# Performance work log

Hardware: AMD Instinct MI355X
Metric: run time of the kernel (lower is better)

Reference implementation:

```python
import jax, jax.numpy as jnp
import numpy as np

B, SEQ, DIM = 2, 4096, 1024
E, S = 8, 512          # num_slots = seq_len // num_experts
HID = 4 * DIM          # FeedForward hidden: dim * mult
SCALE = DIM ** 0.5     # RMSNorm scale


def rmsnorm(x, gamma):
    # matches F.normalize(x, dim=-1) * dim**0.5 * gamma (eps=1e-12 clamp on the norm)
    n = jnp.linalg.norm(x, axis=-1, keepdims=True)
    return x / jnp.maximum(n, 1e-12) * SCALE * gamma


def setup_inputs() -> dict:
    key = jax.random.key(0)
    ks = jax.random.split(key, 4)
    w_init = lambda k, shape: jax.random.normal(k, shape, dtype=jnp.float32) * 0.02
    return {
        "x": jax.random.normal(ks[0], (B, SEQ, DIM), dtype=jnp.float32),
        "norm_gamma": jnp.ones((DIM,), jnp.float32),
        "slot_norm_gamma": jnp.ones((DIM,), jnp.float32),
        "slot_embeds": jax.random.normal(ks[1], (E, S, DIM), dtype=jnp.float32),
        "w1": w_init(ks[2], (E, DIM, HID)),
        "b1": jnp.zeros((E, HID), jnp.float32),
        "w2": w_init(ks[3], (E, HID, DIM)),
        "b2": jnp.zeros((E, DIM), jnp.float32),
    }


def reference(x, norm_gamma, slot_norm_gamma, slot_embeds, w1, b1, w2, b2):
    xn = rmsnorm(x, norm_gamma)                 # [b, n, d]
    sn = rmsnorm(slot_embeds, slot_norm_gamma)  # [e, s, d]

    logits = jnp.einsum('bnd,esd->bnes', xn, sn)                   # [b, n, e, s]
    dispatch = jax.nn.softmax(logits, axis=1)                      # softmax over tokens n
    b, n, e, s = logits.shape
    combine = jax.nn.softmax(logits.reshape(b, n, e * s), axis=-1) # softmax over (e s)

    slots = jnp.einsum('bnd,bnes->besd', xn, dispatch)             # [b, e, s, d]

    # per-expert FeedForward: Linear -> GELU(exact) -> Linear (dropout=0)
    h = jnp.einsum('besd,edh->besh', slots, w1) + b1[None, :, None, :]
    h = jax.nn.gelu(h, approximate=False)
    eo = jnp.einsum('besh,ehd->besd', h, w2) + b2[None, :, None, :]

    eo = eo.reshape(b, e * s, DIM)                                 # [b, (e s), d]
    out = jnp.einsum('bmd,bnm->bnd', eo, combine)                  # [b, n, d]
    return out
```

## Files before the change

kernel.cpp:

```cpp
#include <hip/hip_runtime.h>
#include <math.h>

#define SEQ    4096
#define DIM    1024
#define NEXP   8
#define NSLOT  512
#define ES     4096
#define HID    4096
#define NB     2
#define RMS_SCALE 32.0f

typedef __attribute__((ext_vector_type(4))) float f32x4;
typedef __attribute__((ext_vector_type(8))) short bf16x8;
typedef __attribute__((ext_vector_type(4))) unsigned short us4;

__device__ __forceinline__ unsigned short f2bf(float f) {
    unsigned u = __float_as_uint(f);
    u += 0x7fff + ((u >> 16) & 1);
    return (unsigned short)(u >> 16);
}
__device__ __forceinline__ float bf2f(unsigned short h) {
    return __uint_as_float(((unsigned)h) << 16);
}
__device__ __forceinline__ float gelu_exact(float x) {
    return 0.5f * x * (1.0f + erff(x * 0.70710678118654752f));
}

#define GLOAD_LDS16(gp, lp) \
    __builtin_amdgcn_global_load_lds((const __attribute__((address_space(1))) void*)(gp), \
                                     (__attribute__((address_space(3))) void*)(lp), 16, 0, 0)

__device__ __forceinline__ unsigned ldsoff(const void* p) {
    return (unsigned)(size_t)(const __attribute__((address_space(3))) void*)p;
}

#define DSR(dst, base, off) asm volatile("ds_read_b128 %0, %1 offset:" off : "=v"(dst) : "v"(base))
#define VM(n) asm volatile("s_waitcnt vmcnt(" #n ")" ::: "memory")
#define BAR __builtin_amdgcn_s_barrier()
#define SCB __builtin_amdgcn_sched_barrier(0)

#define PH_OPEN  SCB; BAR; asm volatile("s_waitcnt lgkmcnt(0)" ::: "memory"); SCB; \
                 __builtin_amdgcn_s_setprio(1);
#define PH_CLOSE __builtin_amdgcn_s_setprio(0); SCB;

__global__ void rmsnorm_split(const float* __restrict__ in, const float* __restrict__ gamma,
                              unsigned short* __restrict__ outc) {
    int row = blockIdx.x;
    int t = threadIdx.x;
    float4 v = reinterpret_cast<const float4*>(in + (size_t)row * DIM)[t];
    float ss = v.x*v.x + v.y*v.y + v.z*v.z + v.w*v.w;
    #pragma unroll
    for (int off = 32; off >= 1; off >>= 1) ss += __shfl_down(ss, off, 64);
    __shared__ float red[4];
    if ((t & 63) == 0) red[t >> 6] = ss;
    __syncthreads();
    float inv = RMS_SCALE / fmaxf(sqrtf(red[0] + red[1] + red[2] + red[3]), 1e-12f);
    float4 g = reinterpret_cast<const float4*>(gamma)[t];
    float f[4] = {v.x*inv*g.x, v.y*inv*g.y, v.z*inv*g.z, v.w*inv*g.w};
    us4 hv, lv;
    #pragma unroll
    for (int q = 0; q < 4; ++q) {
        unsigned short h = f2bf(f[q]);
        hv[q] = h;
        lv[q] = f2bf(f[q] - bf2f(h));
    }
    unsigned short* rb = outc + (size_t)row * 2048;
    *reinterpret_cast<us4*>(&rb[t*4]) = hv;
    *reinterpret_cast<us4*>(&rb[1024 + t*4]) = lv;
}

__global__ void rowmax_reduce(const float* __restrict__ pM, float* __restrict__ rmax) {
    int row = blockIdx.x * 256 + threadIdx.x;
    float m = -INFINITY;
    for (int p = 0; p < 64; ++p) m = fmaxf(m, pM[(size_t)p*8192 + row]);
    rmax[row] = m;
}
__global__ void colmax_reduce(const float* __restrict__ pM, float* __restrict__ cmax) {
    int col = blockIdx.x * 256 + threadIdx.x;
    int b = blockIdx.y;
    float m = -INFINITY;
    for (int p = b*32; p < b*32 + 32; ++p) m = fmaxf(m, pM[(size_t)p*4096 + col]);
    cmax[b*4096 + col] = m;
}
__global__ void sum_reduce(const float* __restrict__ pS, float* __restrict__ sinv) {
    int fl = blockIdx.x * 256 + threadIdx.x;
    float s = 0.f;
    for (int p = 0; p < 128; ++p) s += pS[(size_t)p*8192 + fl];
    sinv[fl] = 1.0f / s;
}

__global__ void make_weights(const float* __restrict__ logits,
                             const float* __restrict__ cmax, const float* __restrict__ rmax,
                             unsigned short* __restrict__ comb, unsigned short* __restrict__ dispT,
                             float* __restrict__ rowpS, float* __restrict__ colpS) {
    int b = blockIdx.z;
    const float* L = logits + (size_t)b * SEQ * ES;
    int n0 = blockIdx.y * 32, e0 = blockIdx.x * 32;
    int t = threadIdx.x;
    int r = t >> 3, c4 = (t & 7) * 4;
    __shared__ unsigned short tile[32][36];
    float4 v = *reinterpret_cast<const float4*>(&L[(size_t)(n0 + r) * ES + e0 + c4]);
    float rm = rmax[b*SEQ + n0 + r];
    float vv[4] = {v.x, v.y, v.z, v.w};
    us4 cb;
    float rs = 0.f;
    #pragma unroll
    for (int q = 0; q < 4; ++q) {
        cb[q] = f2bf(__expf(vv[q] - rm));
        rs += bf2f(cb[q]);
        float dv = __expf(vv[q] - cmax[b*ES + e0 + c4 + q]);
        tile[c4 + q][r] = f2bf(dv);
    }
    *reinterpret_cast<us4*>(&comb[(size_t)b*SEQ*ES + (size_t)(n0 + r)*ES + e0 + c4]) = cb;
    rs += __shfl_xor(rs, 1, 64);
    rs += __shfl_xor(rs, 2, 64);
    rs += __shfl_xor(rs, 4, 64);
    if ((t & 7) == 0)
        rowpS[(size_t)blockIdx.x * 8192 + b*SEQ + n0 + r] = rs;
    __syncthreads();
    us4 o = *reinterpret_cast<us4*>(&tile[t >> 3][(t & 7) * 4]);
    *reinterpret_cast<us4*>(&dispT[(size_t)b*ES*SEQ + (size_t)(e0 + (t >> 3))*SEQ + n0 + (t & 7)*4]) = o;
    float cs = bf2f(o[0]) + bf2f(o[1]) + bf2f(o[2]) + bf2f(o[3]);
    cs += __shfl_xor(cs, 1, 64);
    cs += __shfl_xor(cs, 2, 64);
    cs += __shfl_xor(cs, 4, 64);
    if ((t & 7) == 0)
        colpS[(size_t)blockIdx.y * 8192 + b*ES + e0 + (t >> 3)] = cs;
}

__global__ void transpose_b16(const unsigned short* __restrict__ src, unsigned short* __restrict__ dst,
                              int sld, int dld, long sStride, long dStride) {
    int z = blockIdx.z;
    const unsigned short* S = src + (size_t)z * sStride;
    unsigned short* D = dst + (size_t)z * dStride;
    int r0 = blockIdx.y * 32, c0 = blockIdx.x * 32;
    int t = threadIdx.x;
    __shared__ unsigned short tile[32][36];
    us4 v = *reinterpret_cast<const us4*>(&S[(size_t)(r0 + (t>>3)) * sld + c0 + (t&7)*4]);
    #pragma unroll
    for (int q = 0; q < 4; ++q) tile[(t&7)*4 + q][t>>3] = v[q];
    __syncthreads();
    us4 o = *reinterpret_cast<us4*>(&tile[t >> 3][(t & 7) * 4]);
    *reinterpret_cast<us4*>(&D[(size_t)(c0 + (t>>3)) * dld + r0 + (t&7)*4]) = o;
}

__global__ void transpose_f32_b16(const float* __restrict__ src, unsigned short* __restrict__ dst,
                                  int sld, int dld, long sStride, long dStride) {
    int z = blockIdx.z;
    const float* S = src + (size_t)z * sStride;
    unsigned short* D = dst + (size_t)z * dStride;
    int r0 = blockIdx.y * 32, c0 = blockIdx.x * 32;
    int t = threadIdx.x;
    __shared__ unsigned short tile[32][36];
    float4 v = *reinterpret_cast<const float4*>(&S[(size_t)(r0 + (t>>3)) * sld + c0 + (t&7)*4]);
    float vv[4] = {v.x, v.y, v.z, v.w};
    #pragma unroll
    for (int q = 0; q < 4; ++q) tile[(t&7)*4 + q][t>>3] = f2bf(vv[q]);
    __syncthreads();
    us4 o = *reinterpret_cast<us4*>(&tile[t >> 3][(t & 7) * 4]);
    *reinterpret_cast<us4*>(&D[(size_t)(c0 + (t>>3)) * dld + r0 + (t&7)*4]) = o;
}

template<int EPI, int OM, int STATS, int SPLIT>
__global__ __launch_bounds__(512, 2)
void mfma_gemm256(const unsigned short* __restrict__ A, const unsigned short* __restrict__ B,
                  void* __restrict__ Cv, const float* __restrict__ bias,
                  int N, int K, int lda, int ldb, int ldc,
                  long aStride, long bStride, long cStride, int bMod,
                  float* __restrict__ rowpM, float* __restrict__ colpM) {
    __shared__ unsigned short lds[65536];
    const int t = threadIdx.x;
    const int lane = t & 63, wave = t >> 6;
    const int wr = wave >> 2, wc = wave & 3;
    const int z = blockIdx.z, zb = z % bMod;
    const unsigned short* Ab = A + (size_t)z * aStride;
    const unsigned short* Bb = B + (size_t)zb * bStride;
    const int gx = gridDim.x;
    int flat = blockIdx.x + blockIdx.y * gx;
    const int cpx = (gx * gridDim.y) >> 3;
    flat = (flat & 7) * cpx + (flat >> 3);
    const int m0 = (flat / gx) * 256, n0 = (flat % gx) * 256;

    const int sr = t >> 3;
    const int sg = (t & 7) ^ (sr & 7);
    const unsigned short* gA = Ab + (size_t)(m0 + sr) * lda + sg * 8;
    const unsigned short* gB = Bb + (size_t)(n0 + sr) * ldb + sg * 8;
    unsigned short* ldsw = lds + wave * 512;

    const int lr = lane & 15, lk = lane >> 4;
    const unsigned sw0 = (unsigned)(((lk)     ^ (lr & 7)) << 4);
    const unsigned sw1 = (unsigned)(((4 + lk) ^ (lr & 7)) << 4);
    const unsigned l0  = ldsoff(lds);
    const unsigned arow = (unsigned)((wr*128 + lr) * 128);
    const unsigned brow = (unsigned)((wc*64  + lr) * 128);
    const unsigned ab00 = l0 + arow + sw0,          ab10 = l0 + arow + sw1;
    const unsigned bb00 = l0 + 32768 + brow + sw0,  bb10 = l0 + 32768 + brow + sw1;
    const unsigned ab01 = ab00 + 65536, ab11 = ab10 + 65536;
    const unsigned bb01 = bb00 + 65536, bb11 = bb10 + 65536;

    #define KOA(tt) ((size_t)((SPLIT && (tt) >= 16) ? ((tt)-16)*64 : (tt)*64))
    #define KOB(tt) ((size_t)((SPLIT && (tt) >= 32) ? ((tt)-32)*64 : (tt)*64))

    #define STAGE_A(buf, half, tt) do { \
        const unsigned short* _g = gA + (size_t)((half)*128) * lda + KOA(tt); \
        unsigned short* _l = ldsw + (buf)*32768 + (half)*8192; \
        GLOAD_LDS16(_g, _l); \
        GLOAD_LDS16(_g + (size_t)64*lda, _l + 4096); } while(0)
    #define STAGE_B(buf, half, tt) do { \
        const unsigned short* _g = gB + (size_t)((half)*128) * ldb + KOB(tt); \
        unsigned short* _l = ldsw + (buf)*32768 + 16384 + (half)*8192; \
        GLOAD_LDS16(_g, _l); \
        GLOAD_LDS16(_g + (size_t)64*ldb, _l + 4096); } while(0)

    #define MFMA16(MB, CN) \
        _Pragma("unroll") \
        for (int m = 0; m < 4; ++m) { \
            _Pragma("unroll") \
            for (int n = 0; n < 2; ++n) { \
                acc[(MB)+m][(CN)+n] = __builtin_amdgcn_mfma_f32_16x16x32_bf16(a0[m], b0[(CN)+n], acc[(MB)+m][(CN)+n], 0, 0, 0); \
                acc[(MB)+m][(CN)+n] = __builtin_amdgcn_mfma_f32_16x16x32_bf16(a1[m], b1[(CN)+n], acc[(MB)+m][(CN)+n], 0, 0, 0); \
            } \
        }

    f32x4 acc[8][4] = {};
    bf16x8 a0[4], a1[4], b0[4], b1[4];
    const int NT = K / 64;

    STAGE_B(0, 0, 0); STAGE_B(0, 1, 0);
    STAGE_A(0, 0, 0); STAGE_A(0, 1, 0);
    STAGE_B(1, 0, 1); STAGE_B(1, 1, 1);
    VM(4); BAR;

    for (int tt = 0; tt < NT; tt += 2) {
        const bool pf = (tt + 2 < NT);
        DSR(a0[0], ab00, "0");    DSR(a0[1], ab00, "2048");
        DSR(a0[2], ab00, "4096"); DSR(a0[3], ab00, "6144");
        DSR(a1[0], ab10, "0");    DSR(a1[1], ab10, "2048");
        DSR(a1[2], ab10, "4096"); DSR(a1[3], ab10, "6144");
        DSR(b0[0], bb00, "0");    DSR(b0[1], bb00, "2048");
        DSR(b1[0], bb10, "0");    DSR(b1[1], bb10, "2048");
        STAGE_A(1, 0, tt+1);
        PH_OPEN MFMA16(0, 0) PH_CLOSE
        BAR;
        DSR(b0[2], bb00, "4096"); DSR(b0[3], bb00, "6144");
        DSR(b1[2], bb10, "4096"); DSR(b1[3], bb10, "6144");
        STAGE_A(1, 1, tt+1);
        PH_OPEN MFMA16(0, 2) PH_CLOSE
        BAR;
        DSR(a0[0], ab00, "8192");  DSR(a0[1], ab00, "10240");
        DSR(a0[2], ab00, "12288"); DSR(a0[3], ab00, "14336");
        DSR(a1[0], ab10, "8192");  DSR(a1[1], ab10, "10240");
        DSR(a1[2], ab10, "12288"); DSR(a1[3], ab10, "14336");
        if (pf) STAGE_B(0, 0, tt+2);
        PH_OPEN MFMA16(4, 0) PH_CLOSE
        BAR;
        if (pf) STAGE_B(0, 1, tt+2);
        PH_OPEN MFMA16(4, 2) PH_CLOSE
        if (pf) { VM(4); } else { VM(0); }
        BAR;
        DSR(a0[0], ab01, "0");    DSR(a0[1], ab01, "2048");
        DSR(a0[2], ab01, "4096"); DSR(a0[3], ab01, "6144");
        DSR(a1[0], ab11, "0");    DSR(a1[1], ab11, "2048");
        DSR(a1[2], ab11, "4096"); DSR(a1[3], ab11, "6144");
        DSR(b0[0], bb01, "0");    DSR(b0[1], bb01, "2048");
        DSR(b1[0], bb11, "0");    DSR(b1[1], bb11, "2048");
        if (pf) STAGE_A(0, 0, tt+2);
        PH_OPEN MFMA16(0, 0) PH_CLOSE
        BAR;
        DSR(b0[2], bb01, "4096"); DSR(b0[3], bb01, "6144");
        DSR(b1[2], bb11, "4096"); DSR(b1[3], bb11, "6144");
        if (pf) STAGE_A(0, 1, tt+2);
        PH_OPEN MFMA16(0, 2) PH_CLOSE
        BAR;
        DSR(a0[0], ab01, "8192");  DSR(a0[1], ab01, "10240");
        DSR(a0[2], ab01, "12288"); DSR(a0[3], ab01, "14336");
        DSR(a1[0], ab11, "8192");  DSR(a1[1], ab11, "10240");
        DSR(a1[2], ab11, "12288"); DSR(a1[3], ab11, "14336");
        if (pf) STAGE_B(1, 0, tt+3);
        PH_OPEN MFMA16(4, 0) PH_CLOSE
        BAR;
        if (pf) STAGE_B(1, 1, tt+3);
        PH_OPEN MFMA16(4, 2) PH_CLOSE
        if (pf) { VM(4); } else { VM(0); }
        BAR;
    }

    if (STATS) {
        #pragma unroll
        for (int f = 0; f < 8; ++f) {
            #pragma unroll
            for (int r = 0; r < 4; ++r) {
                float m = fmaxf(fmaxf(acc[f][0][r], acc[f][1][r]), fmaxf(acc[f][2][r], acc[f][3][r]));
                #pragma unroll
                for (int msk = 1; msk <= 8; msk <<= 1) m = fmaxf(m, __shfl_xor(m, msk, 64));
                if ((lane & 15) == 0) {
                    int row = m0 + wr*128 + f*16 + (lane>>4)*4 + r;
                    int slot = (n0 >> 6) + wc;
                    rowpM[(size_t)slot*8192 + row] = m;
                }
            }
        }
        #pragma unroll
        for (int n = 0; n < 4; ++n) {
            float m = -INFINITY;
            #pragma unroll
            for (int f = 0; f < 8; ++f)
                #pragma unroll
                for (int r = 0; r < 4; ++r) m = fmaxf(m, acc[f][n][r]);
            m = fmaxf(m, __shfl_xor(m, 16, 64));
            m = fmaxf(m, __shfl_xor(m, 32, 64));
            if ((lane >> 4) == 0) {
                int col = n0 + wc*64 + n*16 + lane;
                int slot = (m0 >> 7) + wr;
                colpM[(size_t)slot*4096 + col] = m;
            }
        }
    }

    const float* bz = (EPI != 0) ? bias + (size_t)zb * N : nullptr;
    long coff = (long)z * cStride;
    int rbase = (lane >> 4) * 4;
    int cbase = lane & 15;
    #pragma unroll
    for (int f = 0; f < 8; ++f) {
        #pragma unroll
        for (int n = 0; n < 4; ++n) {
            int col  = n0 + wc*64 + n*16 + cbase;
            int row0 = m0 + wr*128 + f*16 + rbase;
            float bv = (EPI != 0) ? bz[col] : 0.f;
            float vals[4];
            #pragma unroll
            for (int r = 0; r < 4; ++r) {
                float v = acc[f][n][r] + bv;
                if (EPI == 2) v = gelu_exact(v);
                vals[r] = v;
            }
            if (OM == 0) {
                float* C = (float*)Cv + coff;
                #pragma unroll
                for (int r = 0; r < 4; ++r) C[(size_t)(row0 + r) * ldc + col] = vals[r];
            } else {
                unsigned short* C = (unsigned short*)Cv + coff;
                #pragma unroll
                for (int r = 0; r < 4; ++r) C[(size_t)(row0 + r) * ldc + col] = f2bf(vals[r]);
            }
        }
    }
    #undef STAGE_A
    #undef STAGE_B
    #undef MFMA16
    #undef KOA
    #undef KOB
}

template<int EPI, int OM, int SC>
__global__ __launch_bounds__(512, 2)
void mfma_gemmX(const unsigned short* __restrict__ A, const unsigned short* __restrict__ B,
                void* __restrict__ Cv, const float* __restrict__ bias,
                int N, int K, int lda, int ldb, int ldc,
                long aStride, long bStride, long cStride, long cStrideE, int bMod,
                const float* __restrict__ svec) {
    __shared__ unsigned short lds[49152];
    const int t = threadIdx.x;
    const int lane = t & 63, wave = t >> 6;
    const int wr = wave >> 2, wc = wave & 3;
    const int z = blockIdx.z, zb = z % bMod;
    const unsigned short* Ab = A + (size_t)z * aStride;
    const unsigned short* Bb = B + (size_t)zb * bStride;
    const int gx = gridDim.x;
    int flat = blockIdx.x + blockIdx.y * gx;
    const int cpx = (gx * gridDim.y) >> 3;
    flat = (flat & 7) * cpx + (flat >> 3);
    const int m0 = (flat / gx) * 256, n0 = (flat % gx) * 128;

    const int sr = t >> 3;
    const int sg = (t & 7) ^ (sr & 7);
    const unsigned short* gA = Ab + (size_t)(m0 + sr) * lda + sg * 8;
    const unsigned short* gB = Bb + (size_t)(n0 + sr) * ldb + sg * 8;
    unsigned short* ldsw = lds + wave * 512;

    const int lr = lane & 15, lk = lane >> 4;
    const unsigned g0 = (unsigned)(((lk)     ^ (lr & 7)) << 4);
    const unsigned g1 = (unsigned)(((4 + lk) ^ (lr & 7)) << 4);
    const unsigned l0 = ldsoff(lds);
    const unsigned arow = (unsigned)((wr*64 + lr) * 128);
    const unsigned brow = (unsigned)((wc*32 + lr) * 128);
    const unsigned ax00 = l0 + arow + g0,          ax10 = l0 + arow + g1;
    const unsigned bx00 = l0 + 32768 + brow + g0,  bx10 = l0 + 32768 + brow + g1;
    const unsigned ax01 = ax00 + 49152, ax11 = ax10 + 49152;
    const unsigned bx01 = bx00 + 49152, bx11 = bx10 + 49152;

    #define STAGE_AX(buf, quad, tt) do { \
        const unsigned short* _g = gA + (size_t)((quad)*64) * lda + (tt)*64; \
        unsigned short* _l = ldsw + (buf)*24576 + (quad)*8192; \
        GLOAD_LDS16(_g, _l); \
        GLOAD_LDS16(_g + (size_t)128*lda, _l + 4096); } while(0)
    #define STAGE_BX(buf, tt) do { \
        const unsigned short* _g = gB + (tt)*64; \
        unsigned short* _l = ldsw + (buf)*24576 + 16384; \
        GLOAD_LDS16(_g, _l); \
        GLOAD_LDS16(_g + (size_t)64*ldb, _l + 4096); } while(0)

    #define MFMA8(MB, AR, BR) \
        _Pragma("unroll") \
        for (int m = 0; m < 4; ++m) { \
            _Pragma("unroll") \
            for (int n = 0; n < 2; ++n) { \
                acc[(MB)+m][n] = __builtin_amdgcn_mfma_f32_16x16x32_bf16(AR[m], BR[n], acc[(MB)+m][n], 0, 0, 0); \
            } \
        }

    f32x4 acc[8][2] = {};
    bf16x8 a0[4], a1[4], b0[2], b1[2];
    const int NT = K / 64;

    STAGE_AX(0, 0, 0); STAGE_BX(0, 0); STAGE_AX(0, 1, 0);
    STAGE_AX(1, 0, 1); STAGE_BX(1, 1);
    VM(0); BAR;

    for (int tt = 0; tt < NT; tt += 2) {
        const bool pf2 = (tt + 2 < NT);
        const bool pf3 = (tt + 3 < NT);
        DSR(a0[0], ax00, "0");    DSR(a0[1], ax00, "2048");
        DSR(a0[2], ax00, "4096"); DSR(a0[3], ax00, "6144");
        DSR(b0[0], bx00, "0");    DSR(b0[1], bx00, "2048");
        STAGE_AX(1, 1, tt+1);
        PH_OPEN MFMA8(0, a0, b0) PH_CLOSE
        BAR;
        DSR(a1[0], ax10, "0");    DSR(a1[1], ax10, "2048");
        DSR(a1[2], ax10, "4096"); DSR(a1[3], ax10, "6144");
        DSR(b1[0], bx10, "0");    DSR(b1[1], bx10, "2048");
        PH_OPEN MFMA8(0, a1, b1) PH_CLOSE
        BAR;
        DSR(a0[0], ax00, "16384"); DSR(a0[1], ax00, "18432");
        DSR(a0[2], ax00, "20480"); DSR(a0[3], ax00, "22528");
        if (pf2) STAGE_AX(0, 0, tt+2);
        PH_OPEN MFMA8(4, a0, b0) PH_CLOSE
        BAR;
        DSR(a1[0], ax10, "16384"); DSR(a1[1], ax10, "18432");
        DSR(a1[2], ax10, "20480"); DSR(a1[3], ax10, "22528");
        if (pf2) STAGE_BX(0, tt+2);
        PH_OPEN MFMA8(4, a1, b1) PH_CLOSE
        if (pf2) { VM(4); } else { VM(0); }
        BAR;
        DSR(a0[0], ax01, "0");    DSR(a0[1], ax01, "2048");
        DSR(a0[2], ax01, "4096"); DSR(a0[3], ax01, "6144");
        DSR(b0[0], bx01, "0");    DSR(b0[1], bx01, "2048");
        if (pf2) STAGE_AX(0, 1, tt+2);
        PH_OPEN MFMA8(0, a0, b0) PH_CLOSE
        BAR;
        DSR(a1[0], ax11, "0");    DSR(a1[1], ax11, "2048");
        DSR(a1[2], ax11, "4096"); DSR(a1[3], ax11, "6144");
        DSR(b1[0], bx11, "0");    DSR(b1[1], bx11, "2048");
        PH_OPEN MFMA8(0, a1, b1) PH_CLOSE
        BAR;
        DSR(a0[0], ax01, "16384"); DSR(a0[1], ax01, "18432");
        DSR(a0[2], ax01, "20480"); DSR(a0[3], ax01, "22528");
        if (pf3) STAGE_AX(1, 0, tt+3);
        PH_OPEN MFMA8(4, a0, b0) PH_CLOSE
        BAR;
        DSR(a1[0], ax11, "16384"); DSR(a1[1], ax11, "18432");
        DSR(a1[2], ax11, "20480"); DSR(a1[3], ax11, "22528");
        if (pf3) STAGE_BX(1, tt+3);
        PH_OPEN MFMA8(4, a1, b1) PH_CLOSE
        if (pf3) { VM(4); } else { VM(0); }
        BAR;
    }

    const float* bz = (EPI != 0) ? bias + (size_t)zb * N : nullptr;
    const float* sv = SC ? svec + (size_t)z * 4096 : nullptr;
    long coff = (long)z * cStride + (long)zb * cStrideE;
    int rbase = (lane >> 4) * 4;
    int cbase = lane & 15;
    #pragma unroll
    for (int f = 0; f < 8; ++f) {
        #pragma unroll
        for (int n = 0; n < 2; ++n) {
            int col  = n0 + wc*32 + n*16 + cbase;
            int row0 = m0 + wr*128 + f*16 + rbase;
            float bv = (EPI != 0) ? bz[col] : 0.f;
            float vals[4];
            #pragma unroll
            for (int r = 0; r < 4; ++r) {
                float v = acc[f][n][r] + bv;
                if (SC) v *= sv[row0 + r];
                if (EPI == 2) v = gelu_exact(v);
                vals[r] = v;
            }
            if (OM == 0) {
                float* C = (float*)Cv + coff;
                #pragma unroll
                for (int r = 0; r < 4; ++r) C[(size_t)(row0 + r) * ldc + col] = vals[r];
            } else if (OM == 1) {
                unsigned short* C = (unsigned short*)Cv + coff;
                #pragma unroll
                for (int r = 0; r < 4; ++r) C[(size_t)(row0 + r) * ldc + col] = f2bf(vals[r]);
            } else {
                unsigned short* C = (unsigned short*)Cv + coff;
                us4 o;
                #pragma unroll
                for (int r = 0; r < 4; ++r) o[r] = f2bf(vals[r]);
                *reinterpret_cast<us4*>(&C[(size_t)col * ldc + row0]) = o;
            }
        }
    }
    #undef STAGE_AX
    #undef STAGE_BX
    #undef MFMA8
}

extern "C" void kernel_launch(void* const* d_in, const int* in_sizes, int n_in,
                              void* d_out, int out_size, void* d_ws, size_t ws_size,
                              hipStream_t stream) {
    const float* x    = (const float*)d_in[0];
    const float* ng   = (const float*)d_in[1];
    const float* sg   = (const float*)d_in[2];
    const float* semb = (const float*)d_in[3];
    const float* w1   = (const float*)d_in[4];
    const float* b1   = (const float*)d_in[5];
    const float* w2   = (const float*)d_in[6];
    const float* b2   = (const float*)d_in[7];
    float* out = (float*)d_out;

    char* base = (char*)d_ws;
    unsigned short* Acat  = (unsigned short*)(base);
    unsigned short* Bcat  = (unsigned short*)(base + 33554432);
    unsigned short* dispT = (unsigned short*)(base);
    unsigned short* w2T   = (unsigned short*)(base);
    float*          logits= (float*)(base + 75497472);
    unsigned short* hbuf  = (unsigned short*)(base + 75497472);
    unsigned short* w1T   = (unsigned short*)(base + 142606336);
    unsigned short* xnT   = (unsigned short*)(base + 209715200);
    unsigned short* comb  = (unsigned short*)(base + 226492416);
    unsigned short* slots = (unsigned short*)(base + 293601280);
    unsigned short* eoT   = (unsigned short*)(base + 293601280);
    float* rowpM = (float*)(base + 226492416);
    float* colpM = rowpM + 64*8192;
    float* rmax  = (float*)(base + 310378496);
    float* rinv  = rmax + 8192;
    float* cmax  = rinv + 8192;
    float* cinv  = cmax + 8192;
    float* rowpS = cinv + 8192;
    float* colpS = rowpS + 128*8192;

    rmsnorm_split<<<NB*SEQ, 256, 0, stream>>>(x, ng, Acat);
    rmsnorm_split<<<NEXP*NSLOT, 256, 0, stream>>>(semb, sg, Bcat);

    transpose_b16<<<dim3(DIM/32, SEQ/32, NB), 256, 0, stream>>>(
        Acat, xnT, 2048, SEQ, (long)SEQ*2048, (long)DIM*SEQ);

    mfma_gemm256<0,0,1,1><<<dim3(ES/256, (NB*SEQ)/256, 1), 512, 0, stream>>>(
        Acat, Bcat, logits, nullptr, ES, 3072, 2048, 2048, ES,
        0L, 0L, 0L, 1, rowpM, colpM);

    rowmax_reduce<<<32, 256, 0, stream>>>(rowpM, rmax);
    colmax_reduce<<<dim3(16, 2), 256, 0, stream>>>(colpM, cmax);

    make_weights<<<dim3(ES/32, SEQ/32, NB), 256, 0, stream>>>(
        logits, cmax, rmax, comb, dispT, rowpS, colpS);

    sum_reduce<<<32, 256, 0, stream>>>(rowpS, rinv);
    sum_reduce<<<32, 256, 0, stream>>>(colpS, cinv);

    transpose_f32_b16<<<dim3(HID/32, DIM/32, NEXP), 256, 0, stream>>>(
        w1, w1T, HID, DIM, (long)DIM*HID, (long)HID*DIM);

    mfma_gemmX<0,1,1><<<dim3(DIM/128, ES/256, NB), 512, 0, stream>>>(
        dispT, xnT, slots, nullptr, DIM, SEQ, SEQ, SEQ, DIM,
        (long)ES*SEQ, (long)DIM*SEQ, (long)ES*DIM, 0L, NB, cinv);

    transpose_f32_b16<<<dim3(DIM/32, HID/32, NEXP), 256, 0, stream>>>(
        w2, w2T, DIM, HID, (long)HID*DIM, (long)DIM*HID);

    mfma_gemm256<2,1,0,0><<<dim3(HID/256, NSLOT/256, NB*NEXP), 512, 0, stream>>>(
        slots, w1T, hbuf, b1, HID, DIM, DIM, DIM, HID,
        (long)NSLOT*DIM, (long)HID*DIM, (long)NSLOT*HID, NEXP,
        nullptr, nullptr);

    mfma_gemmX<1,2,0><<<dim3(DIM/128, NSLOT/256, NB*NEXP), 512, 0, stream>>>(
        hbuf, w2T, eoT, b2, DIM, HID, HID, HID, ES,
        (long)NSLOT*HID, (long)DIM*HID, (long)(DIM*ES/NEXP), (long)(NSLOT - DIM*ES/NEXP), NEXP,
        nullptr);

    mfma_gemmX<0,0,1><<<dim3(DIM/128, SEQ/256, NB), 512, 0, stream>>>(
        comb, eoT, out, nullptr, DIM, ES, ES, ES, DIM,
        (long)SEQ*ES, (long)DIM*ES, (long)SEQ*DIM, 0L, NB, rinv);
}
```

Baseline: 700.9 us.

## Switch GEMMs from bf16 to fp16 and shorten split-precision logits K

Replaces bf16 storage and MFMA instructions with fp16 throughout, and changes the logits GEMM's split-precision scheme. The x operand is still split into hi and lo halves, but the slot operand now duplicates its hi part, so K drops from 3072 to 2048 (x_hi·s_hi + x_lo·s_hi). This removes a third of the logits GEMM work by relying on fp16's extra mantissa bits for slot embeddings. The trade-off is fp16's narrower exponent range, which risks overflow or underflow in the exp values, hidden activations and weights.

```diff
diff --git a/kernel.cpp b/kernel.cpp
--- a/kernel.cpp
+++ b/kernel.cpp
@@ -11,16 +11,18 @@
 #define RMS_SCALE 32.0f
 
 typedef __attribute__((ext_vector_type(4))) float f32x4;
-typedef __attribute__((ext_vector_type(8))) short bf16x8;
+typedef __attribute__((ext_vector_type(8))) _Float16 f16x8;
 typedef __attribute__((ext_vector_type(4))) unsigned short us4;
 
-__device__ __forceinline__ unsigned short f2bf(float f) {
-    unsigned u = __float_as_uint(f);
-    u += 0x7fff + ((u >> 16) & 1);
-    return (unsigned short)(u >> 16);
-}
-__device__ __forceinline__ float bf2f(unsigned short h) {
-    return __uint_as_float(((unsigned)h) << 16);
+__device__ __forceinline__ unsigned short f2h(float f) {
+    union { _Float16 h; unsigned short u; } c;
+    c.h = (_Float16)f;
+    return c.u;
+}
+__device__ __forceinline__ float h2f(unsigned short u) {
+    union { unsigned short u; _Float16 h; } c;
+    c.u = u;
+    return (float)c.h;
 }
 __device__ __forceinline__ float gelu_exact(float x) {
     return 0.5f * x * (1.0f + erff(x * 0.70710678118654752f));
@@ -43,6 +45,7 @@
                  __builtin_amdgcn_s_setprio(1);
 #define PH_CLOSE __builtin_amdgcn_s_setprio(0); SCB;
 
+template<int ORDER>
 __global__ void rmsnorm_split(const float* __restrict__ in, const float* __restrict__ gamma,
                               unsigned short* __restrict__ outc) {
     int row = blockIdx.x;
@@ -60,9 +63,9 @@
     us4 hv, lv;
     #pragma unroll
     for (int q = 0; q < 4; ++q) {
-        unsigned short h = f2bf(f[q]);
+        unsigned short h = f2h(f[q]);
         hv[q] = h;
-        lv[q] = f2bf(f[q] - bf2f(h));
+        lv[q] = (ORDER == 0) ? f2h(f[q] - h2f(h)) : h;
     }
     unsigned short* rb = outc + (size_t)row * 2048;
     *reinterpret_cast<us4*>(&rb[t*4]) = hv;
@@ -106,10 +109,10 @@
     float rs = 0.f;
     #pragma unroll
     for (int q = 0; q < 4; ++q) {
-        cb[q] = f2bf(__expf(vv[q] - rm));
-        rs += bf2f(cb[q]);
+        cb[q] = f2h(__expf(vv[q] - rm));
+        rs += h2f(cb[q]);
         float dv = __expf(vv[q] - cmax[b*ES + e0 + c4 + q]);
-        tile[c4 + q][r] = f2bf(dv);
+        tile[c4 + q][r] = f2h(dv);
     }
     *reinterpret_cast<us4*>(&comb[(size_t)b*SEQ*ES + (size_t)(n0 + r)*ES + e0 + c4]) = cb;
     rs += __shfl_xor(rs, 1, 64);
@@ -120,7 +123,7 @@
     __syncthreads();
     us4 o = *reinterpret_cast<us4*>(&tile[t >> 3][(t & 7) * 4]);
     *reinterpret_cast<us4*>(&dispT[(size_t)b*ES*SEQ + (size_t)(e0 + (t >> 3))*SEQ + n0 + (t & 7)*4]) = o;
-    float cs = bf2f(o[0]) + bf2f(o[1]) + bf2f(o[2]) + bf2f(o[3]);
+    float cs = h2f(o[0]) + h2f(o[1]) + h2f(o[2]) + h2f(o[3]);
     cs += __shfl_xor(cs, 1, 64);
     cs += __shfl_xor(cs, 2, 64);
     cs += __shfl_xor(cs, 4, 64);
@@ -144,7 +147,7 @@
     *reinterpret_cast<us4*>(&D[(size_t)(c0 + (t>>3)) * dld + r0 + (t&7)*4]) = o;
 }
 
-__global__ void transpose_f32_b16(const float* __restrict__ src, unsigned short* __restrict__ dst,
+__global__ void transpose_f32_h16(const float* __restrict__ src, unsigned short* __restrict__ dst,
                                   int sld, int dld, long sStride, long dStride) {
     int z = blockIdx.z;
     const float* S = src + (size_t)z * sStride;
@@ -155,13 +158,13 @@
     float4 v = *reinterpret_cast<const float4*>(&S[(size_t)(r0 + (t>>3)) * sld + c0 + (t&7)*4]);
     float vv[4] = {v.x, v.y, v.z, v.w};
     #pragma unroll
-    for (int q = 0; q < 4; ++q) tile[(t&7)*4 + q][t>>3] = f2bf(vv[q]);
+    for (int q = 0; q < 4; ++q) tile[(t&7)*4 + q][t>>3] = f2h(vv[q]);
     __syncthreads();
     us4 o = *reinterpret_cast<us4*>(&tile[t >> 3][(t & 7) * 4]);
     *reinterpret_cast<us4*>(&D[(size_t)(c0 + (t>>3)) * dld + r0 + (t&7)*4]) = o;
 }
 
-template<int EPI, int OM, int STATS, int SPLIT>
+template<int EPI, int OM, int STATS>
 __global__ __launch_bounds__(512, 2)
 void mfma_gemm256(const unsigned short* __restrict__ A, const unsigned short* __restrict__ B,
                   void* __restrict__ Cv, const float* __restrict__ bias,
@@ -198,16 +201,13 @@
     const unsigned ab01 = ab00 + 65536, ab11 = ab10 + 65536;
     const unsigned bb01 = bb00 + 65536, bb11 = bb10 + 65536;
 
-    #define KOA(tt) ((size_t)((SPLIT && (tt) >= 16) ? ((tt)-16)*64 : (tt)*64))
-    #define KOB(tt) ((size_t)((SPLIT && (tt) >= 32) ? ((tt)-32)*64 : (tt)*64))
-
     #define STAGE_A(buf, half, tt) do { \
-        const unsigned short* _g = gA + (size_t)((half)*128) * lda + KOA(tt); \
+        const unsigned short* _g = gA + (size_t)((half)*128) * lda + (size_t)(tt)*64; \
         unsigned short* _l = ldsw + (buf)*32768 + (half)*8192; \
         GLOAD_LDS16(_g, _l); \
         GLOAD_LDS16(_g + (size_t)64*lda, _l + 4096); } while(0)
     #define STAGE_B(buf, half, tt) do { \
-        const unsigned short* _g = gB + (size_t)((half)*128) * ldb + KOB(tt); \
+        const unsigned short* _g = gB + (size_t)((half)*128) * ldb + (size_t)(tt)*64; \
         unsigned short* _l = ldsw + (buf)*32768 + 16384 + (half)*8192; \
         GLOAD_LDS16(_g, _l); \
         GLOAD_LDS16(_g + (size_t)64*ldb, _l + 4096); } while(0)
@@ -217,13 +217,13 @@
         for (int m = 0; m < 4; ++m) { \
             _Pragma("unroll") \
             for (int n = 0; n < 2; ++n) { \
-                acc[(MB)+m][(CN)+n] = __builtin_amdgcn_mfma_f32_16x16x32_bf16(a0[m], b0[(CN)+n], acc[(MB)+m][(CN)+n], 0, 0, 0); \
-                acc[(MB)+m][(CN)+n] = __builtin_amdgcn_mfma_f32_16x16x32_bf16(a1[m], b1[(CN)+n], acc[(MB)+m][(CN)+n], 0, 0, 0); \
+                acc[(MB)+m][(CN)+n] = __builtin_amdgcn_mfma_f32_16x16x32_f16(a0[m], b0[(CN)+n], acc[(MB)+m][(CN)+n], 0, 0, 0); \
+                acc[(MB)+m][(CN)+n] = __builtin_amdgcn_mfma_f32_16x16x32_f16(a1[m], b1[(CN)+n], acc[(MB)+m][(CN)+n], 0, 0, 0); \
             } \
         }
 
     f32x4 acc[8][4] = {};
-    bf16x8 a0[4], a1[4], b0[4], b1[4];
+    f16x8 a0[4], a1[4], b0[4], b1[4];
     const int NT = K / 64;
 
     STAGE_B(0, 0, 0); STAGE_B(0, 1, 0);
@@ -342,15 +342,13 @@
             } else {
                 unsigned short* C = (unsigned short*)Cv + coff;
                 #pragma unroll
-                for (int r = 0; r < 4; ++r) C[(size_t)(row0 + r) * ldc + col] = f2bf(vals[r]);
+                for (int r = 0; r < 4; ++r) C[(size_t)(row0 + r) * ldc + col] = f2h(vals[r]);
             }
         }
     }
     #undef STAGE_A
     #undef STAGE_B
     #undef MFMA16
-    #undef KOA
-    #undef KOB
 }
 
 template<int EPI, int OM, int SC>
@@ -391,12 +389,12 @@
     const unsigned bx01 = bx00 + 49152, bx11 = bx10 + 49152;
 
     #define STAGE_AX(buf, quad, tt) do { \
-        const unsigned short* _g = gA + (size_t)((quad)*64) * lda + (tt)*64; \
+        const unsigned short* _g = gA + (size_t)((quad)*64) * lda + (size_t)(tt)*64; \
         unsigned short* _l = ldsw + (buf)*24576 + (quad)*8192; \
         GLOAD_LDS16(_g, _l); \
         GLOAD_LDS16(_g + (size_t)128*lda, _l + 4096); } while(0)
     #define STAGE_BX(buf, tt) do { \
-        const unsigned short* _g = gB + (tt)*64; \
+        const unsigned short* _g = gB + (size_t)(tt)*64; \
         unsigned short* _l = ldsw + (buf)*24576 + 16384; \
         GLOAD_LDS16(_g, _l); \
         GLOAD_LDS16(_g + (size_t)64*ldb, _l + 4096); } while(0)
@@ -406,12 +404,12 @@
         for (int m = 0; m < 4; ++m) { \
             _Pragma("unroll") \
             for (int n = 0; n < 2; ++n) { \
-                acc[(MB)+m][n] = __builtin_amdgcn_mfma_f32_16x16x32_bf16(AR[m], BR[n], acc[(MB)+m][n], 0, 0, 0); \
+                acc[(MB)+m][n] = __builtin_amdgcn_mfma_f32_16x16x32_f16(AR[m], BR[n], acc[(MB)+m][n], 0, 0, 0); \
             } \
         }
 
     f32x4 acc[8][2] = {};
-    bf16x8 a0[4], a1[4], b0[2], b1[2];
+    f16x8 a0[4], a1[4], b0[2], b1[2];
     const int NT = K / 64;
 
     STAGE_AX(0, 0, 0); STAGE_BX(0, 0); STAGE_AX(0, 1, 0);
@@ -494,12 +492,12 @@
             } else if (OM == 1) {
                 unsigned short* C = (unsigned short*)Cv + coff;
                 #pragma unroll
-                for (int r = 0; r < 4; ++r) C[(size_t)(row0 + r) * ldc + col] = f2bf(vals[r]);
+                for (int r = 0; r < 4; ++r) C[(size_t)(row0 + r) * ldc + col] = f2h(vals[r]);
             } else {
                 unsigned short* C = (unsigned short*)Cv + coff;
                 us4 o;
                 #pragma unroll
-                for (int r = 0; r < 4; ++r) o[r] = f2bf(vals[r]);
+                for (int r = 0; r < 4; ++r) o[r] = f2h(vals[r]);
                 *reinterpret_cast<us4*>(&C[(size_t)col * ldc + row0]) = o;
             }
         }
@@ -543,14 +541,14 @@
     float* rowpS = cinv + 8192;
     float* colpS = rowpS + 128*8192;
 
-    rmsnorm_split<<<NB*SEQ, 256, 0, stream>>>(x, ng, Acat);
-    rmsnorm_split<<<NEXP*NSLOT, 256, 0, stream>>>(semb, sg, Bcat);
+    rmsnorm_split<0><<<NB*SEQ, 256, 0, stream>>>(x, ng, Acat);
+    rmsnorm_split<1><<<NEXP*NSLOT, 256, 0, stream>>>(semb, sg, Bcat);
 
     transpose_b16<<<dim3(DIM/32, SEQ/32, NB), 256, 0, stream>>>(
         Acat, xnT, 2048, SEQ, (long)SEQ*2048, (long)DIM*SEQ);
 
-    mfma_gemm256<0,0,1,1><<<dim3(ES/256, (NB*SEQ)/256, 1), 512, 0, stream>>>(
-        Acat, Bcat, logits, nullptr, ES, 3072, 2048, 2048, ES,
+    mfma_gemm256<0,0,1><<<dim3(ES/256, (NB*SEQ)/256, 1), 512, 0, stream>>>(
+        Acat, Bcat, logits, nullptr, ES, 2048, 2048, 2048, ES,
         0L, 0L, 0L, 1, rowpM, colpM);
 
     rowmax_reduce<<<32, 256, 0, stream>>>(rowpM, rmax);
@@ -562,17 +560,17 @@
     sum_reduce<<<32, 256, 0, stream>>>(rowpS, rinv);
     sum_reduce<<<32, 256, 0, stream>>>(colpS, cinv);
 
-    transpose_f32_b16<<<dim3(HID/32, DIM/32, NEXP), 256, 0, stream>>>(
+    transpose_f32_h16<<<dim3(HID/32, DIM/32, NEXP), 256, 0, stream>>>(
         w1, w1T, HID, DIM, (long)DIM*HID, (long)HID*DIM);
 
     mfma_gemmX<0,1,1><<<dim3(DIM/128, ES/256, NB), 512, 0, stream>>>(
         dispT, xnT, slots, nullptr, DIM, SEQ, SEQ, SEQ, DIM,
         (long)ES*SEQ, (long)DIM*SEQ, (long)ES*DIM, 0L, NB, cinv);
 
-    transpose_f32_b16<<<dim3(DIM/32, HID/32, NEXP), 256, 0, stream>>>(
+    transpose_f32_h16<<<dim3(DIM/32, HID/32, NEXP), 256, 0, stream>>>(
         w2, w2T, DIM, HID, (long)HID*DIM, (long)DIM*HID);
 
-    mfma_gemm256<2,1,0,0><<<dim3(HID/256, NSLOT/256, NB*NEXP), 512, 0, stream>>>(
+    mfma_gemm256<2,1,0><<<dim3(HID/256, NSLOT/256, NB*NEXP), 512, 0, stream>>>(
         slots, w1T, hbuf, b1, HID, DIM, DIM, DIM, HID,
         (long)NSLOT*DIM, (long)HID*DIM, (long)NSLOT*HID, NEXP,
         nullptr, nullptr);
```

Measured after the change: 655.0 us. -6.5%, faster.
